# Kernel tuning notes

Hardware: AMD Instinct MI355X
Metric: run time of the kernel (lower is better)

## Reference

```python
import jax, jax.numpy as jnp
import numpy as np

N_CLS = 3

def _conv(x, w, b):
    # 3x3 'same' conv, NHWC / HWIO
    return jax.lax.conv_general_dilated(
        x, w, window_strides=(1, 1), padding='SAME',
        dimension_numbers=('NHWC', 'HWIO', 'NHWC')) + b


def setup_inputs() -> dict:
    key = jax.random.key(0)
    ks = jax.random.split(key, 24)
    B, H, W, C0 = 4, 512, 512, 32   # decoder outputs['0']
    C4 = 256                         # encoder features['4'] channels
    f32 = jnp.float32
    p = lambda k, s: jax.random.normal(k, s, f32) * 0.05
    inp = {
        'x0': jax.random.normal(ks[0], (B, H, W, C0), f32),
        'f4': jax.random.normal(ks[1], (B, 32, 32, C4), f32),
        # offset head: BatchConv2D(64) x2 (BN folded) + Conv2D(2*n_cls)
        'Wo1': p(ks[2], (3, 3, C0, 64)), 'bo1': jnp.zeros((64,), f32),
        'Wo2': p(ks[3], (3, 3, 64, 64)), 'bo2': jnp.zeros((64,), f32),
        'Wo3': p(ks[4], (3, 3, 64, 2 * N_CLS)), 'bo3': jnp.zeros((2 * N_CLS,), f32),
        # weight head: BatchConv2D(64) x2 + Conv2D(n_cls)
        'Ww1': p(ks[5], (3, 3, C0, 64)), 'bw1': jnp.zeros((64,), f32),
        'Ww2': p(ks[6], (3, 3, 64, 64)), 'bw2': jnp.zeros((64,), f32),
        'Ww3': p(ks[7], (3, 3, 64, N_CLS)), 'bw3': jnp.zeros((N_CLS,), f32),
        # classification head: GAP -> Dense(128) -> Dense(128) -> Dense(n_cls, softmax)
        'Wc1': p(ks[8], (C4, 128)), 'bc1': jnp.zeros((128,), f32),
        'Wc2': p(ks[9], (128, 128)), 'bc2': jnp.zeros((128,), f32),
        'Wc3': p(ks[10], (128, N_CLS)), 'bc3': jnp.zeros((N_CLS,), f32),
    }
    return inp


def reference(x0, f4, Wo1, bo1, Wo2, bo2, Wo3, bo3,
              Ww1, bw1, Ww2, bw2, Ww3, bw3,
              Wc1, bc1, Wc2, bc2, Wc3, bc3):
    # offset head -> [B,H,W,2*n_cls]
    h = jax.nn.relu(_conv(x0, Wo1, bo1))
    h = jax.nn.relu(_conv(h, Wo2, bo2))
    offsets_full = _conv(h, Wo3, bo3)
    # weight head -> [B,H,W,n_cls]
    g = jax.nn.relu(_conv(x0, Ww1, bw1))
    g = jax.nn.relu(_conv(g, Ww2, bw2))
    weights_full = _conv(g, Ww3, bw3)
    # classification head on features['4']
    gap = jnp.mean(f4, axis=(1, 2))                 # [B,C4]
    z = jax.nn.relu(gap @ Wc1 + bc1)
    z = jax.nn.relu(z @ Wc2 + bc2)
    pred_cls = jax.nn.softmax(z @ Wc3 + bc3, axis=-1)  # [B,n_cls]
    # inference path: cls = argmax(pred_cls)
    cls = jnp.argmax(pred_cls, axis=-1).astype(jnp.int32)  # [B]
    # tf.gather(offsets, stack([cls*2, cls*2+1],-1), axis=-1, batch_dims=1)
    idx2 = jnp.stack([cls * 2, cls * 2 + 1], axis=-1)[:, None, None, :]  # [B,1,1,2]
    offsets = jnp.take_along_axis(
        offsets_full, jnp.broadcast_to(idx2, offsets_full.shape[:3] + (2,)), axis=-1)
    # tf.gather(weights, cls[:,None], axis=-1, batch_dims=1)
    idx1 = cls[:, None, None, None]
    weights = jnp.take_along_axis(
        weights_full, jnp.broadcast_to(idx1, weights_full.shape[:3] + (1,)), axis=-1)
    return offsets, weights, pred_cls
```

## Files before the change

kernel.cpp:

```cpp
#include <hip/hip_runtime.h>
#include <hip/hip_bf16.h>
#include <math.h>

typedef __attribute__((ext_vector_type(8))) short short8;
typedef __attribute__((ext_vector_type(4))) short short4v;
typedef __attribute__((ext_vector_type(4))) float floatx4;
typedef unsigned short ushort_t;
typedef unsigned int uint_t;

__device__ __forceinline__ ushort_t f2bf(float x) {
    uint_t u = __float_as_uint(x);
    uint_t r = (u + 0x7fffu + ((u >> 16) & 1u)) >> 16;
    return (ushort_t)r;
}
__device__ __forceinline__ short4v pack4(float a, float b, float c, float d) {
    union { __hip_bfloat162 h; uint_t u; } lo, hi;
    lo.h = __float22bfloat162_rn(make_float2(a, b));
    hi.h = __float22bfloat162_rn(make_float2(c, d));
    short4v r;
    r[0] = (short)(lo.u & 0xffffu); r[1] = (short)(lo.u >> 16);
    r[2] = (short)(hi.u & 0xffffu); r[3] = (short)(hi.u >> 16);
    return r;
}
__device__ __forceinline__ short8 pack8(float4 v0, float4 v1) {
    short4v lo = pack4(v0.x, v0.y, v0.z, v0.w);
    short4v hi = pack4(v1.x, v1.y, v1.z, v1.w);
    short8 pk;
    pk[0] = lo[0]; pk[1] = lo[1]; pk[2] = lo[2]; pk[3] = lo[3];
    pk[4] = hi[0]; pk[5] = hi[1]; pk[6] = hi[2]; pk[7] = hi[3];
    return pk;
}

__global__ void prep_all(const float* __restrict__ W1a, const float* __restrict__ W2a,
                         const float* __restrict__ W1b, const float* __restrict__ W2b,
                         const float* __restrict__ W3a, const float* __restrict__ W3b,
                         ushort_t* __restrict__ wt, ushort_t* __restrict__ w3t,
                         const float* __restrict__ f4, float* __restrict__ part) {
    __shared__ float4 red[256];
    int bi = blockIdx.x, t = threadIdx.x;
    if (bi < 432) {
        int i = bi * 256 + t;
        const float* W; int off; int C;
        if (i < 18432)      { W = W1a; off = i;         C = 32; }
        else if (i < 55296) { W = W2a; off = i - 18432; C = 64; }
        else if (i < 73728) { W = W1b; off = i - 55296; C = 32; }
        else                { W = W2b; off = i - 73728; C = 64; }
        int pt = C * 64;
        int tap = off / pt, rem = off - tap * pt;
        int k4 = rem >> 9, rem2 = rem & 511;
        int co = rem2 >> 3, j = rem2 & 7;
        int ci = k4 * 8 + j;
        wt[i] = f2bf(W[(size_t)(tap * C + ci) * 64 + co]);
    } else if (bi < 648) {
        int i = (bi - 432) * 256 + t;
        int branch = i / 27648; int r = i - branch * 27648;
        int cls = r / 9216; int r2 = r - cls * 9216;
        int t2 = r2 >> 9; int r3 = r2 & 511;
        int qq = r3 >> 7; int r4 = r3 & 127;
        int ch = r4 >> 3; int j = r4 & 7;
        int tap = t2 >> 1, kh = t2 & 1;
        int ci = kh * 32 + qq * 8 + j;
        int NCH = branch ? 1 : 2, C3 = branch ? 3 : 6;
        const float* W3 = branch ? W3b : W3a;
        ushort_t v = 0;
        if (ch < NCH) v = f2bf(W3[(size_t)(tap * 64 + ci) * C3 + cls * NCH + ch]);
        w3t[i] = v;
    } else {
        int g = bi - 648;
        int c = g & 7, b = g >> 3;
        int ci4 = t & 63, po = t >> 6;
        const float* f = f4 + ((size_t)b * 1024 + c * 128) * 256;
        float4 s = {0, 0, 0, 0};
        for (int i = 0; i < 32; ++i) {
            float4 v = *(const float4*)&f[(size_t)(i * 4 + po) * 256 + ci4 * 4];
            s.x += v.x; s.y += v.y; s.z += v.z; s.w += v.w;
        }
        red[t] = s;
        __syncthreads();
        if (t < 64) {
            float4 a = red[t], b2 = red[64 + t], c2 = red[128 + t], d2 = red[192 + t];
            float4 gg;
            gg.x = a.x + b2.x + c2.x + d2.x;
            gg.y = a.y + b2.y + c2.y + d2.y;
            gg.z = a.z + b2.z + c2.z + d2.z;
            gg.w = a.w + b2.w + c2.w + d2.w;
            *(float4*)&part[((b * 8 + c) << 8) + t * 4] = gg;
        }
    }
}

__global__ void cls_finish(const float* __restrict__ part,
                           const float* __restrict__ Wc1, const float* __restrict__ bc1,
                           const float* __restrict__ Wc2, const float* __restrict__ bc2,
                           const float* __restrict__ Wc3, const float* __restrict__ bc3,
                           float* __restrict__ pred_out, int* __restrict__ cls_out) {
    int b = blockIdx.x;
    int t = threadIdx.x;
    __shared__ float gap[256];
    __shared__ float z1[128];
    __shared__ float z2[128];
    __shared__ float lg[3];
    float s = 0.f;
    for (int c = 0; c < 8; ++c) s += part[((b * 8 + c) << 8) + t];
    gap[t] = s * (1.0f / 1024.0f);
    __syncthreads();
    if (t < 128) {
        float a = bc1[t];
        for (int i = 0; i < 256; ++i) a += gap[i] * Wc1[i * 128 + t];
        z1[t] = fmaxf(a, 0.f);
    }
    __syncthreads();
    if (t < 128) {
        float a = bc2[t];
        for (int i = 0; i < 128; ++i) a += z1[i] * Wc2[i * 128 + t];
        z2[t] = fmaxf(a, 0.f);
    }
    __syncthreads();
    if (t < 3) {
        float a = bc3[t];
        for (int i = 0; i < 128; ++i) a += z2[i] * Wc3[i * 3 + t];
        lg[t] = a;
    }
    __syncthreads();
    if (t == 0) {
        float m = fmaxf(lg[0], fmaxf(lg[1], lg[2]));
        float e0 = expf(lg[0] - m), e1 = expf(lg[1] - m), e2 = expf(lg[2] - m);
        float ssum = e0 + e1 + e2;
        pred_out[b * 3 + 0] = e0 / ssum;
        pred_out[b * 3 + 1] = e1 / ssum;
        pred_out[b * 3 + 2] = e2 / ssum;
        int idx = 0; float best = lg[0];
        if (lg[1] > best) { best = lg[1]; idx = 1; }
        if (lg[2] > best) { best = lg[2]; idx = 2; }
        cls_out[b] = idx;
    }
}

#define X0_E 0
#define X0_KS 2592
#define H1_E 10368
#define H1_KS 2048
#define H2_E 0
#define SF_F 7200
#define LDS_E 26752

__global__ __launch_bounds__(256, 3)
void fused_branch(const float* __restrict__ x0,
                  const ushort_t* __restrict__ W1o_t, const ushort_t* __restrict__ W2o_t,
                  const ushort_t* __restrict__ W1w_t, const ushort_t* __restrict__ W2w_t,
                  const ushort_t* __restrict__ w3t,
                  const float* __restrict__ bo1, const float* __restrict__ bo2,
                  const float* __restrict__ bw1, const float* __restrict__ bw2,
                  const float* __restrict__ bo3, const float* __restrict__ bw3,
                  const int* __restrict__ clsp,
                  float* __restrict__ off_out, float* __restrict__ w_out) {
    __shared__ __align__(16) ushort_t lds[LDS_E];
    float* ldsf = (float*)lds;
    const int t = threadIdx.x;
    const int b = blockIdx.y;
    const int z = blockIdx.z;
    const ushort_t* W1t = z ? W1w_t : W1o_t;
    const ushort_t* W2t = z ? W2w_t : W2o_t;
    const ushort_t* W3T = w3t + z * 27648;
    const float* B1 = z ? bw1 : bo1;
    const float* B2 = z ? bw2 : bo2;
    const float* B3 = z ? bw3 : bo3;
    float* outp = z ? w_out : off_out;
    const int NCH = z ? 1 : 2;

    const int tileY = blockIdx.x / 43, tileX = blockIdx.x - tileY * 43;
    const int ty0 = tileY * 12, tx0 = tileX * 12;
    const bool edge = (tileY == 0) | (tileY == 42) | (tileX == 0) | (tileX == 42);
    const int lane = t & 63, wave = t >> 6;
    const int m = lane & 15, q = lane >> 4;
    const int cls = clsp[b];

    if (!edge) {
        for (int idx = t; idx < 1296; idx += 256) {
            int pix = idx >> 2, qq = idx & 3;
            int py = pix / 18, px = pix - py * 18;
            const float* xp = x0 + (((size_t)b * 512 + (ty0 - 3 + py)) * 512 + (tx0 - 3 + px)) * 32 + qq * 8;
            *(short8*)&lds[X0_E + qq * X0_KS + pix * 8] =
                pack8(*(const float4*)xp, *(const float4*)(xp + 4));
        }
    } else {
        for (int idx = t; idx < 1296; idx += 256) {
            int pix = idx >> 2, qq = idx & 3;
            int py = pix / 18, px = pix - py * 18;
            int gy = ty0 - 3 + py, gx = tx0 - 3 + px;
            float4 v0 = {0, 0, 0, 0}, v1 = {0, 0, 0, 0};
            if ((uint_t)gy < 512u && (uint_t)gx < 512u) {
                const float* xp = x0 + (((size_t)b * 512 + gy) * 512 + gx) * 32 + qq * 8;
                v0 = *(const float4*)xp;
                v1 = *(const float4*)(xp + 4);
            }
            *(short8*)&lds[X0_E + qq * X0_KS + pix * 8] = pack8(v0, v1);
        }
    }
    __syncthreads();

    {
        floatx4 acc[4][4];
#pragma unroll
        for (int mi = 0; mi < 4; ++mi) {
            float4 bb = *(const float4*)&B1[mi * 16 + q * 4];
            floatx4 ib = (floatx4){bb.x, bb.y, bb.z, bb.w};
#pragma unroll
            for (int n = 0; n < 4; ++n) acc[mi][n] = ib;
        }
        const int wsel = q * 512 + m * 8;
        short8 Anow[4];
#pragma unroll
        for (int mi = 0; mi < 4; ++mi)
            Anow[mi] = *(const short8*)&W1t[wsel + mi * 128];

        for (int tap = 0; tap < 9; ++tap) {
            int tn = tap < 8 ? tap + 1 : 8;
            short8 Anext[4];
#pragma unroll
            for (int mi = 0; mi < 4; ++mi)
                Anext[mi] = *(const short8*)&W1t[tn * 2048 + wsel + mi * 128];
            int dy = tap / 3, dx = tap - dy * 3;
            short8 Bx[4];
#pragma unroll
            for (int n = 0; n < 4; ++n) {
                int ptile = n * 4 + wave;
                Bx[n] = *(const short8*)&lds[X0_E + q * X0_KS + ((ptile + dy) * 18 + (m + dx)) * 8];
            }
#pragma unroll
            for (int mi = 0; mi < 4; ++mi)
#pragma unroll
                for (int n = 0; n < 4; ++n)
                    acc[mi][n] = __builtin_amdgcn_mfma_f32_16x16x32_bf16(Anow[mi], Bx[n], acc[mi][n], 0, 0, 0);
#pragma unroll
            for (int mi = 0; mi < 4; ++mi) Anow[mi] = Anext[mi];
        }
        if (!edge) {
#pragma unroll
            for (int mi = 0; mi < 4; ++mi) {
                int ks = mi * 2 + (q >> 1), lo = (q & 1) * 4;
#pragma unroll
                for (int n = 0; n < 4; ++n) {
                    int ptile = n * 4 + wave;
                    floatx4 a = acc[mi][n];
                    *(short4v*)&lds[H1_E + ks * H1_KS + (ptile * 16 + m) * 8 + lo] =
                        pack4(fmaxf(a[0], 0.f), fmaxf(a[1], 0.f), fmaxf(a[2], 0.f), fmaxf(a[3], 0.f));
                }
            }
        } else {
#pragma unroll
            for (int mi = 0; mi < 4; ++mi) {
                int ks = mi * 2 + (q >> 1), lo = (q & 1) * 4;
#pragma unroll
                for (int n = 0; n < 4; ++n) {
                    int ptile = n * 4 + wave;
                    int gy = ty0 - 2 + ptile, gx = tx0 - 2 + m;
                    bool ok = ((uint_t)gy < 512u) && ((uint_t)gx < 512u);
                    floatx4 a = acc[mi][n];
                    float v0 = ok ? fmaxf(a[0], 0.f) : 0.f;
                    float v1 = ok ? fmaxf(a[1], 0.f) : 0.f;
                    float v2 = ok ? fmaxf(a[2], 0.f) : 0.f;
                    float v3 = ok ? fmaxf(a[3], 0.f) : 0.f;
                    *(short4v*)&lds[H1_E + ks * H1_KS + (ptile * 16 + m) * 8 + lo] = pack4(v0, v1, v2, v3);
                }
            }
        }
    }
    __syncthreads();

    {
        floatx4 acc[4][4];
#pragma unroll
        for (int mi = 0; mi < 4; ++mi) {
            float4 bb = *(const float4*)&B2[mi * 16 + q * 4];
            floatx4 ib = (floatx4){bb.x, bb.y, bb.z, bb.w};
#pragma unroll
            for (int n = 0; n < 4; ++n) acc[mi][n] = ib;
        }
        int hb2[4];
#pragma unroll
        for (int n = 0; n < 4; ++n) {
            int p0 = (n * 4 + wave) * 16 + m;
            int pv = p0 < 196 ? p0 : 195;
            int py = pv / 14, px = pv - py * 14;
            hb2[n] = py * 16 + px;
        }
        const int wsel = q * 512 + m * 8;
        short8 Anow[4];
#pragma unroll
        for (int mi = 0; mi < 4; ++mi)
            Anow[mi] = *(const short8*)&W2t[wsel + mi * 128];

        for (int s = 0; s < 18; ++s) {
            int tap = s >> 1, kh = s & 1;
            int sn = s < 17 ? s + 1 : 17;
            short8 Anext[4];
#pragma unroll
            for (int mi = 0; mi < 4; ++mi)
                Anext[mi] = *(const short8*)&W2t[(sn >> 1) * 4096 + ((sn & 1) * 4) * 512 + wsel + mi * 128];
            int dy = tap / 3, dx = tap - dy * 3;
            short8 Bx[4];
#pragma unroll
            for (int n = 0; n < 4; ++n)
                Bx[n] = *(const short8*)&lds[H1_E + (kh * 4 + q) * H1_KS + (hb2[n] + dy * 16 + dx) * 8];
#pragma unroll
            for (int mi = 0; mi < 4; ++mi)
#pragma unroll
                for (int n = 0; n < 4; ++n) {
                    int ptile = n * 4 + wave;
                    if (ptile < 13)
                        acc[mi][n] = __builtin_amdgcn_mfma_f32_16x16x32_bf16(Anow[mi], Bx[n], acc[mi][n], 0, 0, 0);
                }
#pragma unroll
            for (int mi = 0; mi < 4; ++mi) Anow[mi] = Anext[mi];
        }
        __syncthreads();
#pragma unroll
        for (int n = 0; n < 4; ++n) {
            int ptile = n * 4 + wave;
            if (ptile >= 13) continue;
            int p = ptile * 16 + m;
            bool pok = p < 196;
            bool ok = pok;
            if (edge) {
                int py = p / 14, px = p - py * 14;
                int gy = ty0 - 1 + py, gx = tx0 - 1 + px;
                ok = pok && ((uint_t)gy < 512u) && ((uint_t)gx < 512u);
            }
#pragma unroll
            for (int mi = 0; mi < 4; ++mi) {
                floatx4 a = acc[mi][n];
                float v0 = ok ? fmaxf(a[0], 0.f) : 0.f;
                float v1 = ok ? fmaxf(a[1], 0.f) : 0.f;
                float v2 = ok ? fmaxf(a[2], 0.f) : 0.f;
                float v3 = ok ? fmaxf(a[3], 0.f) : 0.f;
                if (pok)
                    *(short4v*)&lds[H2_E + p * 72 + mi * 16 + q * 4] = pack4(v0, v1, v2, v3);
            }
        }
    }
    __syncthreads();

    {
        floatx4 acc3[9];
#pragma unroll
        for (int n = 0; n < 9; ++n) acc3[n] = (floatx4){0.f, 0.f, 0.f, 0.f};
        int hb3[9];
#pragma unroll
        for (int n = 0; n < 9; ++n) {
            int p = n * 16 + m;
            int py = p / 12, px = p - py * 12;
            hb3[n] = py * 14 + px;
        }
        const ushort_t* W3c = W3T + cls * 9216;
        for (int t2 = wave; t2 < 18; t2 += 4) {
            int tap = t2 >> 1, kh = t2 & 1;
            int dy = tap / 3, dx = tap - dy * 3;
            short8 Aw = *(const short8*)&W3c[t2 * 512 + q * 128 + m * 8];
#pragma unroll
            for (int n = 0; n < 9; ++n) {
                short8 Bh = *(const short8*)&lds[H2_E + (hb3[n] + dy * 14 + dx) * 72 + kh * 32 + q * 8];
                acc3[n] = __builtin_amdgcn_mfma_f32_16x16x32_bf16(Aw, Bh, acc3[n], 0, 0, 0);
            }
        }
        float* sf = ldsf + SF_F;
        if (q == 0) {
#pragma unroll
            for (int n = 0; n < 9; ++n) {
                float2 v = {acc3[n][0], acc3[n][1]};
                *(float2*)&sf[wave * 288 + n * 32 + m * 2] = v;
            }
        }
    }
    __syncthreads();
    if (t < 144) {
        float* sf = ldsf + SF_F;
        int p = t;
        int base = (p >> 4) * 32 + (p & 15) * 2;
        float a0 = sf[base] + sf[288 + base] + sf[576 + base] + sf[864 + base];
        int py = p / 12, px = p - py * 12;
        int gy = ty0 + py, gx = tx0 + px;
        if (gy < 512 && gx < 512) {
            size_t ob = (((size_t)b * 512 + gy) * 512 + gx) * NCH;
            outp[ob] = a0 + B3[cls * NCH + 0];
            if (NCH == 2) {
                float a1 = sf[base + 1] + sf[288 + base + 1] + sf[576 + base + 1] + sf[864 + base + 1];
                outp[ob + 1] = a1 + B3[cls * NCH + 1];
            }
        }
    }
}

extern "C" void kernel_launch(void* const* d_in, const int* in_sizes, int n_in,
                              void* d_out, int out_size, void* d_ws, size_t ws_size,
                              hipStream_t stream) {
    const float* x0  = (const float*)d_in[0];
    const float* f4  = (const float*)d_in[1];
    const float* Wo1 = (const float*)d_in[2];  const float* bo1 = (const float*)d_in[3];
    const float* Wo2 = (const float*)d_in[4];  const float* bo2 = (const float*)d_in[5];
    const float* Wo3 = (const float*)d_in[6];  const float* bo3 = (const float*)d_in[7];
    const float* Ww1 = (const float*)d_in[8];  const float* bw1 = (const float*)d_in[9];
    const float* Ww2 = (const float*)d_in[10]; const float* bw2 = (const float*)d_in[11];
    const float* Ww3 = (const float*)d_in[12]; const float* bw3 = (const float*)d_in[13];
    const float* Wc1 = (const float*)d_in[14]; const float* bc1 = (const float*)d_in[15];
    const float* Wc2 = (const float*)d_in[16]; const float* bc2 = (const float*)d_in[17];
    const float* Wc3 = (const float*)d_in[18]; const float* bc3 = (const float*)d_in[19];

    float* out = (float*)d_out;
    float* offsets_out = out;
    float* weights_out = out + 2097152;
    float* pred_out    = out + 3145728;

    int* cls_ws = (int*)d_ws;
    ushort_t* wt  = (ushort_t*)((char*)d_ws + 16);
    ushort_t* w3t = (ushort_t*)((char*)d_ws + 221200);
    float* gap_part = (float*)((char*)d_ws + 331792);

    const ushort_t* W1o_t = wt;
    const ushort_t* W2o_t = wt + 18432;
    const ushort_t* W1w_t = wt + 55296;
    const ushort_t* W2w_t = wt + 73728;

    prep_all<<<680, 256, 0, stream>>>(Wo1, Wo2, Ww1, Ww2, Wo3, Ww3, wt, w3t, f4, gap_part);
    cls_finish<<<4, 256, 0, stream>>>(gap_part, Wc1, bc1, Wc2, bc2, Wc3, bc3, pred_out, cls_ws);

    dim3 grid(43 * 43, 4, 2);
    fused_branch<<<grid, 256, 0, stream>>>(x0,
                                           W1o_t, W2o_t, W1w_t, W2w_t, w3t,
                                           bo1, bo2, bw1, bw2,
                                           bo3, bw3,
                                           cls_ws, offsets_out, weights_out);
}
```

Baseline: 613.6 us.

## Process both heads per block, reusing the staged x0 tile, and restructure conv3

The two branch heads now run in one block through an unrolled loop, so the x0 halo tile is loaded and converted to bf16 once instead of twice, and the grid loses its z dimension. The LDS channel-slice strides get padding, presumably to reduce bank conflicts. h2 is stored in a channel-sliced layout that reuses the h1 region. The final conv now splits pixel tiles across waves instead of splitting taps, which removes the cross-wave float reduction in LDS and its extra barrier. The cost is half as many blocks, longer serial work per block, and extra barriers between the two branches.

```diff
diff --git a/kernel.cpp b/kernel.cpp
--- a/kernel.cpp
+++ b/kernel.cpp
@@ -137,12 +137,11 @@
 }
 
 #define X0_E 0
-#define X0_KS 2592
-#define H1_E 10368
-#define H1_KS 2048
-#define H2_E 0
-#define SF_F 7200
-#define LDS_E 26752
+#define X0_KS 2608
+#define H1_E 10432
+#define H1_KS 2064
+#define H2_KS 1616
+#define LDS_E 26944
 
 __global__ __launch_bounds__(256, 3)
 void fused_branch(const float* __restrict__ x0,
@@ -155,19 +154,8 @@
                   const int* __restrict__ clsp,
                   float* __restrict__ off_out, float* __restrict__ w_out) {
     __shared__ __align__(16) ushort_t lds[LDS_E];
-    float* ldsf = (float*)lds;
     const int t = threadIdx.x;
     const int b = blockIdx.y;
-    const int z = blockIdx.z;
-    const ushort_t* W1t = z ? W1w_t : W1o_t;
-    const ushort_t* W2t = z ? W2w_t : W2o_t;
-    const ushort_t* W3T = w3t + z * 27648;
-    const float* B1 = z ? bw1 : bo1;
-    const float* B2 = z ? bw2 : bo2;
-    const float* B3 = z ? bw3 : bo3;
-    float* outp = z ? w_out : off_out;
-    const int NCH = z ? 1 : 2;
-
     const int tileY = blockIdx.x / 43, tileX = blockIdx.x - tileY * 43;
     const int ty0 = tileY * 12, tx0 = tileX * 12;
     const bool edge = (tileY == 0) | (tileY == 42) | (tileX == 0) | (tileX == 42);
@@ -199,195 +187,206 @@
     }
     __syncthreads();
 
-    {
-        floatx4 acc[4][4];
-#pragma unroll
-        for (int mi = 0; mi < 4; ++mi) {
-            float4 bb = *(const float4*)&B1[mi * 16 + q * 4];
-            floatx4 ib = (floatx4){bb.x, bb.y, bb.z, bb.w};
-#pragma unroll
-            for (int n = 0; n < 4; ++n) acc[mi][n] = ib;
-        }
-        const int wsel = q * 512 + m * 8;
-        short8 Anow[4];
-#pragma unroll
-        for (int mi = 0; mi < 4; ++mi)
-            Anow[mi] = *(const short8*)&W1t[wsel + mi * 128];
-
-        for (int tap = 0; tap < 9; ++tap) {
-            int tn = tap < 8 ? tap + 1 : 8;
-            short8 Anext[4];
+#pragma unroll
+    for (int br = 0; br < 2; ++br) {
+        const ushort_t* W1t = br ? W1w_t : W1o_t;
+        const ushort_t* W2t = br ? W2w_t : W2o_t;
+        const ushort_t* W3T = w3t + br * 27648;
+        const float* B1 = br ? bw1 : bo1;
+        const float* B2 = br ? bw2 : bo2;
+        const float* B3 = br ? bw3 : bo3;
+        float* outp = br ? w_out : off_out;
+        const int NCH = br ? 1 : 2;
+
+        {
+            floatx4 acc[4][4];
+#pragma unroll
+            for (int mi = 0; mi < 4; ++mi) {
+                float4 bb = *(const float4*)&B1[mi * 16 + q * 4];
+                floatx4 ib = (floatx4){bb.x, bb.y, bb.z, bb.w};
+#pragma unroll
+                for (int n = 0; n < 4; ++n) acc[mi][n] = ib;
+            }
+            const int wsel = q * 512 + m * 8;
+            short8 Anow[4];
 #pragma unroll
             for (int mi = 0; mi < 4; ++mi)
-                Anext[mi] = *(const short8*)&W1t[tn * 2048 + wsel + mi * 128];
-            int dy = tap / 3, dx = tap - dy * 3;
-            short8 Bx[4];
+                Anow[mi] = *(const short8*)&W1t[wsel + mi * 128];
+
+            for (int tap = 0; tap < 9; ++tap) {
+                int tn = tap < 8 ? tap + 1 : 8;
+                short8 Anext[4];
+#pragma unroll
+                for (int mi = 0; mi < 4; ++mi)
+                    Anext[mi] = *(const short8*)&W1t[tn * 2048 + wsel + mi * 128];
+                int dy = tap / 3, dx = tap - dy * 3;
+                short8 Bx[4];
+#pragma unroll
+                for (int n = 0; n < 4; ++n) {
+                    int ptile = n * 4 + wave;
+                    Bx[n] = *(const short8*)&lds[X0_E + q * X0_KS + ((ptile + dy) * 18 + (m + dx)) * 8];
+                }
+#pragma unroll
+                for (int mi = 0; mi < 4; ++mi)
+#pragma unroll
+                    for (int n = 0; n < 4; ++n)
+                        acc[mi][n] = __builtin_amdgcn_mfma_f32_16x16x32_bf16(Anow[mi], Bx[n], acc[mi][n], 0, 0, 0);
+#pragma unroll
+                for (int mi = 0; mi < 4; ++mi) Anow[mi] = Anext[mi];
+            }
+            if (!edge) {
+#pragma unroll
+                for (int mi = 0; mi < 4; ++mi) {
+                    int ks = mi * 2 + (q >> 1), lo = (q & 1) * 4;
+#pragma unroll
+                    for (int n = 0; n < 4; ++n) {
+                        int ptile = n * 4 + wave;
+                        floatx4 a = acc[mi][n];
+                        *(short4v*)&lds[H1_E + ks * H1_KS + (ptile * 16 + m) * 8 + lo] =
+                            pack4(fmaxf(a[0], 0.f), fmaxf(a[1], 0.f), fmaxf(a[2], 0.f), fmaxf(a[3], 0.f));
+                    }
+                }
+            } else {
+#pragma unroll
+                for (int mi = 0; mi < 4; ++mi) {
+                    int ks = mi * 2 + (q >> 1), lo = (q & 1) * 4;
+#pragma unroll
+                    for (int n = 0; n < 4; ++n) {
+                        int ptile = n * 4 + wave;
+                        int gy = ty0 - 2 + ptile, gx = tx0 - 2 + m;
+                        bool ok = ((uint_t)gy < 512u) && ((uint_t)gx < 512u);
+                        floatx4 a = acc[mi][n];
+                        float v0 = ok ? fmaxf(a[0], 0.f) : 0.f;
+                        float v1 = ok ? fmaxf(a[1], 0.f) : 0.f;
+                        float v2 = ok ? fmaxf(a[2], 0.f) : 0.f;
+                        float v3 = ok ? fmaxf(a[3], 0.f) : 0.f;
+                        *(short4v*)&lds[H1_E + ks * H1_KS + (ptile * 16 + m) * 8 + lo] = pack4(v0, v1, v2, v3);
+                    }
+                }
+            }
+        }
+        __syncthreads();
+
+        {
+            floatx4 acc[4][4];
+#pragma unroll
+            for (int mi = 0; mi < 4; ++mi) {
+                float4 bb = *(const float4*)&B2[mi * 16 + q * 4];
+                floatx4 ib = (floatx4){bb.x, bb.y, bb.z, bb.w};
+#pragma unroll
+                for (int n = 0; n < 4; ++n) acc[mi][n] = ib;
+            }
+            int hb2[4];
+#pragma unroll
+            for (int n = 0; n < 4; ++n) {
+                int p0 = (n * 4 + wave) * 16 + m;
+                int pv = p0 < 196 ? p0 : 195;
+                int py = pv / 14, px = pv - py * 14;
+                hb2[n] = py * 16 + px;
+            }
+            const int wsel = q * 512 + m * 8;
+            short8 Anow[4];
+#pragma unroll
+            for (int mi = 0; mi < 4; ++mi)
+                Anow[mi] = *(const short8*)&W2t[wsel + mi * 128];
+
+            for (int s = 0; s < 18; ++s) {
+                int tap = s >> 1, kh = s & 1;
+                int sn = s < 17 ? s + 1 : 17;
+                short8 Anext[4];
+#pragma unroll
+                for (int mi = 0; mi < 4; ++mi)
+                    Anext[mi] = *(const short8*)&W2t[(sn >> 1) * 4096 + ((sn & 1) * 4) * 512 + wsel + mi * 128];
+                int dy = tap / 3, dx = tap - dy * 3;
+                short8 Bx[4];
+#pragma unroll
+                for (int n = 0; n < 4; ++n)
+                    Bx[n] = *(const short8*)&lds[H1_E + (kh * 4 + q) * H1_KS + (hb2[n] + dy * 16 + dx) * 8];
+#pragma unroll
+                for (int mi = 0; mi < 4; ++mi)
+#pragma unroll
+                    for (int n = 0; n < 4; ++n) {
+                        int ptile = n * 4 + wave;
+                        if (ptile < 13)
+                            acc[mi][n] = __builtin_amdgcn_mfma_f32_16x16x32_bf16(Anow[mi], Bx[n], acc[mi][n], 0, 0, 0);
+                    }
+#pragma unroll
+                for (int mi = 0; mi < 4; ++mi) Anow[mi] = Anext[mi];
+            }
+            __syncthreads();
 #pragma unroll
             for (int n = 0; n < 4; ++n) {
                 int ptile = n * 4 + wave;
-                Bx[n] = *(const short8*)&lds[X0_E + q * X0_KS + ((ptile + dy) * 18 + (m + dx)) * 8];
-            }
-#pragma unroll
-            for (int mi = 0; mi < 4; ++mi)
-#pragma unroll
-                for (int n = 0; n < 4; ++n)
-                    acc[mi][n] = __builtin_amdgcn_mfma_f32_16x16x32_bf16(Anow[mi], Bx[n], acc[mi][n], 0, 0, 0);
-#pragma unroll
-            for (int mi = 0; mi < 4; ++mi) Anow[mi] = Anext[mi];
-        }
-        if (!edge) {
-#pragma unroll
-            for (int mi = 0; mi < 4; ++mi) {
-                int ks = mi * 2 + (q >> 1), lo = (q & 1) * 4;
-#pragma unroll
-                for (int n = 0; n < 4; ++n) {
-                    int ptile = n * 4 + wave;
-                    floatx4 a = acc[mi][n];
-                    *(short4v*)&lds[H1_E + ks * H1_KS + (ptile * 16 + m) * 8 + lo] =
-                        pack4(fmaxf(a[0], 0.f), fmaxf(a[1], 0.f), fmaxf(a[2], 0.f), fmaxf(a[3], 0.f));
-                }
-            }
-        } else {
-#pragma unroll
-            for (int mi = 0; mi < 4; ++mi) {
-                int ks = mi * 2 + (q >> 1), lo = (q & 1) * 4;
-#pragma unroll
-                for (int n = 0; n < 4; ++n) {
-                    int ptile = n * 4 + wave;
-                    int gy = ty0 - 2 + ptile, gx = tx0 - 2 + m;
-                    bool ok = ((uint_t)gy < 512u) && ((uint_t)gx < 512u);
+                if (ptile >= 13) continue;
+                int p = ptile * 16 + m;
+                bool pok = p < 196;
+                bool ok = pok;
+                if (edge) {
+                    int py = p / 14, px = p - py * 14;
+                    int gy = ty0 - 1 + py, gx = tx0 - 1 + px;
+                    ok = pok && ((uint_t)gy < 512u) && ((uint_t)gx < 512u);
+                }
+#pragma unroll
+                for (int mi = 0; mi < 4; ++mi) {
+                    int ks = mi * 2 + (q >> 1), lo = (q & 1) * 4;
                     floatx4 a = acc[mi][n];
                     float v0 = ok ? fmaxf(a[0], 0.f) : 0.f;
                     float v1 = ok ? fmaxf(a[1], 0.f) : 0.f;
                     float v2 = ok ? fmaxf(a[2], 0.f) : 0.f;
                     float v3 = ok ? fmaxf(a[3], 0.f) : 0.f;
-                    *(short4v*)&lds[H1_E + ks * H1_KS + (ptile * 16 + m) * 8 + lo] = pack4(v0, v1, v2, v3);
-                }
-            }
-        }
-    }
-    __syncthreads();
-
-    {
-        floatx4 acc[4][4];
-#pragma unroll
-        for (int mi = 0; mi < 4; ++mi) {
-            float4 bb = *(const float4*)&B2[mi * 16 + q * 4];
-            floatx4 ib = (floatx4){bb.x, bb.y, bb.z, bb.w};
-#pragma unroll
-            for (int n = 0; n < 4; ++n) acc[mi][n] = ib;
-        }
-        int hb2[4];
-#pragma unroll
-        for (int n = 0; n < 4; ++n) {
-            int p0 = (n * 4 + wave) * 16 + m;
-            int pv = p0 < 196 ? p0 : 195;
-            int py = pv / 14, px = pv - py * 14;
-            hb2[n] = py * 16 + px;
-        }
-        const int wsel = q * 512 + m * 8;
-        short8 Anow[4];
-#pragma unroll
-        for (int mi = 0; mi < 4; ++mi)
-            Anow[mi] = *(const short8*)&W2t[wsel + mi * 128];
-
-        for (int s = 0; s < 18; ++s) {
-            int tap = s >> 1, kh = s & 1;
-            int sn = s < 17 ? s + 1 : 17;
-            short8 Anext[4];
-#pragma unroll
-            for (int mi = 0; mi < 4; ++mi)
-                Anext[mi] = *(const short8*)&W2t[(sn >> 1) * 4096 + ((sn & 1) * 4) * 512 + wsel + mi * 128];
-            int dy = tap / 3, dx = tap - dy * 3;
-            short8 Bx[4];
-#pragma unroll
-            for (int n = 0; n < 4; ++n)
-                Bx[n] = *(const short8*)&lds[H1_E + (kh * 4 + q) * H1_KS + (hb2[n] + dy * 16 + dx) * 8];
-#pragma unroll
-            for (int mi = 0; mi < 4; ++mi)
-#pragma unroll
-                for (int n = 0; n < 4; ++n) {
-                    int ptile = n * 4 + wave;
-                    if (ptile < 13)
-                        acc[mi][n] = __builtin_amdgcn_mfma_f32_16x16x32_bf16(Anow[mi], Bx[n], acc[mi][n], 0, 0, 0);
-                }
-#pragma unroll
-            for (int mi = 0; mi < 4; ++mi) Anow[mi] = Anext[mi];
+                    if (pok)
+                        *(short4v*)&lds[H1_E + ks * H2_KS + p * 8 + lo] = pack4(v0, v1, v2, v3);
+                }
+            }
         }
         __syncthreads();
-#pragma unroll
-        for (int n = 0; n < 4; ++n) {
-            int ptile = n * 4 + wave;
-            if (ptile >= 13) continue;
-            int p = ptile * 16 + m;
-            bool pok = p < 196;
-            bool ok = pok;
-            if (edge) {
-                int py = p / 14, px = p - py * 14;
-                int gy = ty0 - 1 + py, gx = tx0 - 1 + px;
-                ok = pok && ((uint_t)gy < 512u) && ((uint_t)gx < 512u);
-            }
-#pragma unroll
-            for (int mi = 0; mi < 4; ++mi) {
-                floatx4 a = acc[mi][n];
-                float v0 = ok ? fmaxf(a[0], 0.f) : 0.f;
-                float v1 = ok ? fmaxf(a[1], 0.f) : 0.f;
-                float v2 = ok ? fmaxf(a[2], 0.f) : 0.f;
-                float v3 = ok ? fmaxf(a[3], 0.f) : 0.f;
-                if (pok)
-                    *(short4v*)&lds[H2_E + p * 72 + mi * 16 + q * 4] = pack4(v0, v1, v2, v3);
-            }
-        }
-    }
-    __syncthreads();
-
-    {
-        floatx4 acc3[9];
-#pragma unroll
-        for (int n = 0; n < 9; ++n) acc3[n] = (floatx4){0.f, 0.f, 0.f, 0.f};
-        int hb3[9];
-#pragma unroll
-        for (int n = 0; n < 9; ++n) {
-            int p = n * 16 + m;
-            int py = p / 12, px = p - py * 12;
-            hb3[n] = py * 14 + px;
-        }
-        const ushort_t* W3c = W3T + cls * 9216;
-        for (int t2 = wave; t2 < 18; t2 += 4) {
-            int tap = t2 >> 1, kh = t2 & 1;
-            int dy = tap / 3, dx = tap - dy * 3;
-            short8 Aw = *(const short8*)&W3c[t2 * 512 + q * 128 + m * 8];
-#pragma unroll
-            for (int n = 0; n < 9; ++n) {
-                short8 Bh = *(const short8*)&lds[H2_E + (hb3[n] + dy * 14 + dx) * 72 + kh * 32 + q * 8];
-                acc3[n] = __builtin_amdgcn_mfma_f32_16x16x32_bf16(Aw, Bh, acc3[n], 0, 0, 0);
-            }
-        }
-        float* sf = ldsf + SF_F;
-        if (q == 0) {
-#pragma unroll
-            for (int n = 0; n < 9; ++n) {
-                float2 v = {acc3[n][0], acc3[n][1]};
-                *(float2*)&sf[wave * 288 + n * 32 + m * 2] = v;
-            }
-        }
-    }
-    __syncthreads();
-    if (t < 144) {
-        float* sf = ldsf + SF_F;
-        int p = t;
-        int base = (p >> 4) * 32 + (p & 15) * 2;
-        float a0 = sf[base] + sf[288 + base] + sf[576 + base] + sf[864 + base];
-        int py = p / 12, px = p - py * 12;
-        int gy = ty0 + py, gx = tx0 + px;
-        if (gy < 512 && gx < 512) {
-            size_t ob = (((size_t)b * 512 + gy) * 512 + gx) * NCH;
-            outp[ob] = a0 + B3[cls * NCH + 0];
-            if (NCH == 2) {
-                float a1 = sf[base + 1] + sf[288 + base + 1] + sf[576 + base + 1] + sf[864 + base + 1];
-                outp[ob + 1] = a1 + B3[cls * NCH + 1];
-            }
-        }
+
+        {
+            floatx4 acc3[3];
+#pragma unroll
+            for (int j = 0; j < 3; ++j) acc3[j] = (floatx4){0.f, 0.f, 0.f, 0.f};
+            int hb3[3];
+#pragma unroll
+            for (int j = 0; j < 3; ++j) {
+                int n = wave + 4 * j;
+                int p = (n < 9 ? n : 8) * 16 + m;
+                int pv = p < 144 ? p : 143;
+                int py = pv / 12, px = pv - py * 12;
+                hb3[j] = py * 14 + px;
+            }
+            const ushort_t* W3c = W3T + cls * 9216;
+            for (int t2 = 0; t2 < 18; ++t2) {
+                int tap = t2 >> 1, kh = t2 & 1;
+                int dy = tap / 3, dx = tap - dy * 3;
+                short8 Aw = *(const short8*)&W3c[t2 * 512 + q * 128 + m * 8];
+#pragma unroll
+                for (int j = 0; j < 3; ++j) {
+                    if (wave + 4 * j < 9) {
+                        short8 Bh = *(const short8*)&lds[H1_E + (kh * 4 + q) * H2_KS + (hb3[j] + dy * 14 + dx) * 8];
+                        acc3[j] = __builtin_amdgcn_mfma_f32_16x16x32_bf16(Aw, Bh, acc3[j], 0, 0, 0);
+                    }
+                }
+            }
+            if (q == 0) {
+#pragma unroll
+                for (int j = 0; j < 3; ++j) {
+                    int n = wave + 4 * j;
+                    if (n < 9) {
+                        int p = n * 16 + m;
+                        if (p < 144) {
+                            int py = p / 12, px = p - py * 12;
+                            int gy = ty0 + py, gx = tx0 + px;
+                            if (((uint_t)gy < 512u) && ((uint_t)gx < 512u)) {
+                                size_t ob = (((size_t)b * 512 + gy) * 512 + gx) * NCH;
+                                outp[ob] = acc3[j][0] + B3[cls * NCH + 0];
+                                if (NCH == 2) outp[ob + 1] = acc3[j][1] + B3[cls * NCH + 1];
+                            }
+                        }
+                    }
+                }
+            }
+        }
+        if (br == 0) __syncthreads();
     }
 }
 
@@ -424,7 +423,7 @@
     prep_all<<<680, 256, 0, stream>>>(Wo1, Wo2, Ww1, Ww2, Wo3, Ww3, wt, w3t, f4, gap_part);
     cls_finish<<<4, 256, 0, stream>>>(gap_part, Wc1, bc1, Wc2, bc2, Wc3, bc3, pred_out, cls_ws);
 
-    dim3 grid(43 * 43, 4, 2);
+    dim3 grid(43 * 43, 4);
     fused_branch<<<grid, 256, 0, stream>>>(x0,
                                            W1o_t, W2o_t, W1w_t, W2w_t, w3t,
                                            bo1, bo2, bw1, bw2,
```

New measurement: 1.015 ms. +65.5%, slower.
